# Performance work log

Hardware: AMD Instinct MI355X
Metric: run time of the kernel (lower is better)

Reference implementation:

```python
import jax, jax.numpy as jnp
import numpy as np

N = 100_000            # nodes
E = 1_600_000          # edges (avg degree 16)
IN, OUT = 64, 16
L1, L2 = 48, 32        # in - floor(k*(in-out)/3) for k=1,2
EDGE_DIM = 16
EPS = 1e-7             # GENConv message epsilon
BN_EPS = 1e-5


def _lin(k, i, o):
    return jax.random.normal(k, (i, o), jnp.float32) / np.float32(np.sqrt(i))


def setup_inputs() -> dict:
    key = jax.random.key(0)
    ks = jax.random.split(key, 16)
    z = lambda d: jnp.zeros((d,), jnp.float32)
    o = lambda d: jnp.ones((d,), jnp.float32)
    return {
        "x": jax.random.normal(ks[0], (N, IN), jnp.float32),
        "edge_index": jax.random.randint(ks[1], (2, E), 0, N),
        "edge_attr": jax.random.normal(ks[2], (E, EDGE_DIM), jnp.float32),
        # GENConv 1 (IN -> L1)
        "w_src1": _lin(ks[3], IN, L1), "b_src1": z(L1),
        "w_edge1": _lin(ks[4], EDGE_DIM, L1), "b_edge1": z(L1),
        "w_m1a": _lin(ks[5], L1, 2 * L1), "b_m1a": z(2 * L1),
        "g1": o(2 * L1), "be1": z(2 * L1),
        "w_m1b": _lin(ks[6], 2 * L1, L1), "b_m1b": z(L1),
        # GENConv 2 (L1 -> L2)
        "w_src2": _lin(ks[7], L1, L2), "b_src2": z(L2),
        "w_edge2": _lin(ks[8], EDGE_DIM, L2), "b_edge2": z(L2),
        "w_m2a": _lin(ks[9], L2, 2 * L2), "b_m2a": z(2 * L2),
        "g2": o(2 * L2), "be2": z(2 * L2),
        "w_m2b": _lin(ks[10], 2 * L2, L2), "b_m2b": z(L2),
        # GCNConv heads (L2 -> OUT)
        "w_mu": _lin(ks[11], L2, OUT), "b_mu": z(OUT),
        "w_ls": _lin(ks[12], L2, OUT), "b_ls": z(OUT),
    }


def _gen_conv(x, src, dst, e_raw, w_src, b_src, w_edge, b_edge,
              w1, b1, g, be, w2, b2):
    """PyG GENConv with softmax aggregation (t=1) and 2-layer MLP w/ batch norm."""
    h = x @ w_src + b_src                      # [N, d] lin_src
    e = e_raw @ w_edge + b_edge                # [E, d] lin_edge
    msg = jax.nn.relu(h[src] + e) + EPS        # [E, d] message
    # per-destination, per-channel softmax aggregation
    mmax = jax.ops.segment_max(msg, dst, num_segments=N)
    mmax = jnp.where(jnp.isfinite(mmax), mmax, 0.0)
    ex = jnp.exp(msg - mmax[dst])
    denom = jax.ops.segment_sum(ex, dst, num_segments=N)
    agg = jax.ops.segment_sum(ex * msg, dst, num_segments=N) / (denom + 1e-16)
    out = agg + h                              # residual with x_dst (lin_src applied)
    # MLP: Linear -> BatchNorm(train stats) -> ReLU -> Linear
    zt = out @ w1 + b1
    zt = (zt - zt.mean(0)) * jax.lax.rsqrt(zt.var(0) + BN_EPS) * g + be
    return jax.nn.relu(zt) @ w2 + b2


def _gcn_conv(x, src, dst, w, b):
    """PyG GCNConv: self-loops + symmetric normalization."""
    loop = jnp.arange(N)
    s = jnp.concatenate([src, loop])
    d = jnp.concatenate([dst, loop])
    deg = jax.ops.segment_sum(jnp.ones(s.shape, x.dtype), d, num_segments=N)
    dinv = jnp.where(deg > 0, jax.lax.rsqrt(deg), 0.0)
    norm = (dinv[s] * dinv[d])[:, None]
    return jax.ops.segment_sum((x @ w)[s] * norm, d, num_segments=N) + b


def reference(x, edge_index, edge_attr,
              w_src1, b_src1, w_edge1, b_edge1, w_m1a, b_m1a, g1, be1, w_m1b, b_m1b,
              w_src2, b_src2, w_edge2, b_edge2, w_m2a, b_m2a, g2, be2, w_m2b, b_m2b,
              w_mu, b_mu, w_ls, b_ls):
    src, dst = edge_index[0], edge_index[1]
    h = jax.nn.relu(_gen_conv(x, src, dst, edge_attr, w_src1, b_src1, w_edge1,
                              b_edge1, w_m1a, b_m1a, g1, be1, w_m1b, b_m1b))
    h = jax.nn.relu(_gen_conv(h, src, dst, edge_attr, w_src2, b_src2, w_edge2,
                              b_edge2, w_m2a, b_m2a, g2, be2, w_m2b, b_m2b))
    mu = _gcn_conv(h, src, dst, w_mu, b_mu)
    logstd = _gcn_conv(h, src, dst, w_ls, b_ls)
    return (mu, logstd)
```

## Files before the change

kernel.cpp:

```cpp
#include <hip/hip_runtime.h>
#include <hip/hip_bf16.h>

typedef unsigned int u32;

#define EPS_MSG 1e-7f
#define BN_EPS  1e-5f

template<int I, int O>
__global__ void k_lin(const float* __restrict__ X, const float* __restrict__ W,
                      const float* __restrict__ B, float* __restrict__ Y,
                      int ldY, int n) {
  __shared__ float Wl[I * O];
  __shared__ float Bl[O];
  for (int t = threadIdx.x; t < I * O; t += blockDim.x) Wl[t] = W[t];
  if (threadIdx.x < O) Bl[threadIdx.x] = B[threadIdx.x];
  __syncthreads();
  int i = blockIdx.x * blockDim.x + threadIdx.x;
  if (i >= n) return;
  float acc[O];
#pragma unroll
  for (int c = 0; c < O; c++) acc[c] = Bl[c];
  const float4* xp = (const float4*)(X + (size_t)i * I);
  for (int q = 0; q < I / 4; q++) {
    float4 v = xp[q];
#pragma unroll
    for (int c = 0; c < O; c++) acc[c] += v.x * Wl[(4 * q + 0) * O + c];
#pragma unroll
    for (int c = 0; c < O; c++) acc[c] += v.y * Wl[(4 * q + 1) * O + c];
#pragma unroll
    for (int c = 0; c < O; c++) acc[c] += v.z * Wl[(4 * q + 2) * O + c];
#pragma unroll
    for (int c = 0; c < O; c++) acc[c] += v.w * Wl[(4 * q + 3) * O + c];
  }
  float* y = Y + (size_t)i * ldY;
#pragma unroll
  for (int c = 0; c < O; c++) y[c] = acc[c];
}

__global__ void k_deg(const int* __restrict__ ei, u32* __restrict__ deg, int E) {
  int e = blockIdx.x * blockDim.x + threadIdx.x;
  if (e < E) atomicAdd(&deg[ei[E + e]], 1u);
}

__global__ void k_scan1(const u32* __restrict__ deg, u32* __restrict__ excl,
                        u32* __restrict__ part, int n) {
  __shared__ u32 sm[256];
  int t = threadIdx.x;
  int base = blockIdx.x * 1024 + t * 4;
  u32 v0 = (base + 0 < n) ? deg[base + 0] : 0u;
  u32 v1 = (base + 1 < n) ? deg[base + 1] : 0u;
  u32 v2 = (base + 2 < n) ? deg[base + 2] : 0u;
  u32 v3 = (base + 3 < n) ? deg[base + 3] : 0u;
  u32 tsum = v0 + v1 + v2 + v3;
  sm[t] = tsum;
  __syncthreads();
  for (int o = 1; o < 256; o <<= 1) {
    u32 v = (t >= o) ? sm[t - o] : 0u;
    __syncthreads();
    sm[t] += v;
    __syncthreads();
  }
  u32 tex = sm[t] - tsum;
  if (t == 255) part[blockIdx.x] = sm[255];
  if (base + 0 < n) excl[base + 0] = tex;
  if (base + 1 < n) excl[base + 1] = tex + v0;
  if (base + 2 < n) excl[base + 2] = tex + v0 + v1;
  if (base + 3 < n) excl[base + 3] = tex + v0 + v1 + v2;
}

__global__ void k_scan2(u32* __restrict__ part, int nb) {
  if (threadIdx.x == 0) {
    u32 acc = 0;
    for (int i = 0; i < nb; i++) { u32 v = part[i]; part[i] = acc; acc += v; }
  }
}

__global__ void k_scan3(u32* __restrict__ rowptr, const u32* __restrict__ part,
                        int n, int E) {
  int i = blockIdx.x * blockDim.x + threadIdx.x;
  if (i < n) rowptr[i] += part[i >> 10];
  if (i == 0) rowptr[n] = (u32)E;
}

__global__ void k_slots(const int* __restrict__ ei, const u32* __restrict__ rowptr,
                        u32* __restrict__ cnt, int* __restrict__ csr_src,
                        int* __restrict__ csr_eid, int E) {
  int e = blockIdx.x * blockDim.x + threadIdx.x;
  if (e >= E) return;
  int s = ei[e], d = ei[E + e];
  u32 slot = rowptr[d] + atomicAdd(&cnt[d], 1u);
  csr_src[slot] = s;
  csr_eid[slot] = e;
}

__global__ void k_gather(const int* __restrict__ csr_eid, const float* __restrict__ ea,
                         float* __restrict__ eaperm, int E) {
  int i = blockIdx.x * blockDim.x + threadIdx.x;
  if (i >= E) return;
  int e = csr_eid[i];
  const float4* p = (const float4*)(ea + (size_t)e * 16);
  float4* q = (float4*)(eaperm + (size_t)i * 16);
  float4 a = p[0], b = p[1], c = p[2], d = p[3];
  q[0] = a; q[1] = b; q[2] = c; q[3] = d;
}

__global__ void k_dinv(const u32* __restrict__ deg, float* __restrict__ dinv, int n) {
  int i = blockIdx.x * blockDim.x + threadIdx.x;
  if (i < n) dinv[i] = rsqrtf((float)(deg[i] + 1u));
}

#define EDGE_DOT(A0,A1,A2,A3) (bias + \
  A0.x * wc[0]  + A0.y * wc[1]  + A0.z * wc[2]  + A0.w * wc[3] + \
  A1.x * wc[4]  + A1.y * wc[5]  + A1.z * wc[6]  + A1.w * wc[7] + \
  A2.x * wc[8]  + A2.y * wc[9]  + A2.z * wc[10] + A2.w * wc[11] + \
  A3.x * wc[12] + A3.y * wc[13] + A3.z * wc[14] + A3.w * wc[15])

template<bool PERM>
__global__ void k_agg48(const u32* __restrict__ rowptr, const int* __restrict__ csr_src,
                        const int* __restrict__ csr_eid, const float* __restrict__ attrs,
                        const float* __restrict__ we, const float* __restrict__ be,
                        const float* __restrict__ h, float* __restrict__ out, int n) {
  int lane = threadIdx.x & 63;
  int node = (blockIdx.x * blockDim.x + threadIdx.x) >> 6;
  if (node >= n) return;
  float wc[16];
#pragma unroll
  for (int k = 0; k < 16; k++) wc[k] = 0.f;
  float bias = 0.f;
  if (lane < 48) {
#pragma unroll
    for (int k = 0; k < 16; k++) wc[k] = we[k * 48 + lane];
    bias = be[lane];
  }
  float hself = (lane < 48) ? h[(size_t)node * 48 + lane] : 0.f;
  u32 b = rowptr[node], t = rowptr[node + 1];
  float den = 0.f, num = 0.f;
  u32 i = b;
  if (PERM) {
    for (; i + 4 <= t; i += 4) {
      int s0 = csr_src[i + 0];
      int s1 = csr_src[i + 1];
      int s2 = csr_src[i + 2];
      int s3 = csr_src[i + 3];
      float hv[4];
      if (lane < 48) {
        hv[0] = h[(size_t)s0 * 48 + lane];
        hv[1] = h[(size_t)s1 * 48 + lane];
        hv[2] = h[(size_t)s2 * 48 + lane];
        hv[3] = h[(size_t)s3 * 48 + lane];
      } else { hv[0] = hv[1] = hv[2] = hv[3] = 0.f; }
#pragma unroll
      for (int j = 0; j < 4; j++) {
        const float4* p = (const float4*)(attrs + (size_t)(i + j) * 16);
        float4 a0 = p[0], a1 = p[1], a2 = p[2], a3 = p[3];
        float ml = EDGE_DOT(a0, a1, a2, a3);
        float m  = fmaxf(hv[j] + ml, 0.f) + EPS_MSG;
        float ex = __expf(m);
        den += ex; num += ex * m;
      }
    }
  }
  for (; i < t; i++) {
    int s = csr_src[i];
    const float4* p = (const float4*)(attrs + (PERM ? (size_t)i : (size_t)csr_eid[i]) * 16);
    float4 a0 = p[0], a1 = p[1], a2 = p[2], a3 = p[3];
    float hvs = (lane < 48) ? h[(size_t)s * 48 + lane] : 0.f;
    float ml = EDGE_DOT(a0, a1, a2, a3);
    float m  = fmaxf(hvs + ml, 0.f) + EPS_MSG;
    float ex = __expf(m);
    den += ex; num += ex * m;
  }
  if (lane < 48)
    out[(size_t)node * 48 + lane] = hself + num / (den + 1e-16f);
}

template<bool PERM>
__global__ void k_agg32(const u32* __restrict__ rowptr, const int* __restrict__ csr_src,
                        const int* __restrict__ csr_eid, const float* __restrict__ attrs,
                        const float* __restrict__ we, const float* __restrict__ be,
                        const float* __restrict__ h, float* __restrict__ out, int n) {
  int c    = threadIdx.x & 31;
  int node = (blockIdx.x * blockDim.x + threadIdx.x) >> 5;
  if (node >= n) return;
  float wc[16];
#pragma unroll
  for (int k = 0; k < 16; k++) wc[k] = we[k * 32 + c];
  float bias  = be[c];
  float hself = h[(size_t)node * 32 + c];
  u32 b = rowptr[node], t = rowptr[node + 1];
  float den = 0.f, num = 0.f;
  u32 i = b;
  if (PERM) {
    for (; i + 4 <= t; i += 4) {
      int s0 = csr_src[i + 0];
      int s1 = csr_src[i + 1];
      int s2 = csr_src[i + 2];
      int s3 = csr_src[i + 3];
      float hv[4];
      hv[0] = h[(size_t)s0 * 32 + c];
      hv[1] = h[(size_t)s1 * 32 + c];
      hv[2] = h[(size_t)s2 * 32 + c];
      hv[3] = h[(size_t)s3 * 32 + c];
#pragma unroll
      for (int j = 0; j < 4; j++) {
        const float4* p = (const float4*)(attrs + (size_t)(i + j) * 16);
        float4 a0 = p[0], a1 = p[1], a2 = p[2], a3 = p[3];
        float ml = EDGE_DOT(a0, a1, a2, a3);
        float m  = fmaxf(hv[j] + ml, 0.f) + EPS_MSG;
        float ex = __expf(m);
        den += ex; num += ex * m;
      }
    }
  }
  for (; i < t; i++) {
    int s = csr_src[i];
    const float4* p = (const float4*)(attrs + (PERM ? (size_t)i : (size_t)csr_eid[i]) * 16);
    float4 a0 = p[0], a1 = p[1], a2 = p[2], a3 = p[3];
    float hvs = h[(size_t)s * 32 + c];
    float ml = EDGE_DOT(a0, a1, a2, a3);
    float m  = fmaxf(hvs + ml, 0.f) + EPS_MSG;
    float ex = __expf(m);
    den += ex; num += ex * m;
  }
  out[(size_t)node * 32 + c] = hself + num / (den + 1e-16f);
}

template<int D>
__global__ void k_ztstats(const float* __restrict__ X, const float* __restrict__ W,
                          const float* __restrict__ B, float* __restrict__ Z1,
                          float* __restrict__ Z2, float* __restrict__ partial, int n) {
  __shared__ float Wl[D * 2 * D];
  __shared__ float Bl[2 * D];
  __shared__ float red[4][4 * D];
  for (int t = threadIdx.x; t < D * 2 * D; t += blockDim.x) Wl[t] = W[t];
  for (int t = threadIdx.x; t < 2 * D; t += blockDim.x) Bl[t] = B[t];
  __syncthreads();
  int i = blockIdx.x * blockDim.x + threadIdx.x;
  bool act = (i < n);
  float acc[2 * D];
#pragma unroll
  for (int c = 0; c < 2 * D; c++) acc[c] = 0.f;
  if (act) {
#pragma unroll
    for (int c = 0; c < 2 * D; c++) acc[c] = Bl[c];
    const float4* xp = (const float4*)(X + (size_t)i * D);
    for (int q = 0; q < D / 4; q++) {
      float4 v = xp[q];
#pragma unroll
      for (int c = 0; c < 2 * D; c++) acc[c] += v.x * Wl[(4 * q + 0) * 2 * D + c];
#pragma unroll
      for (int c = 0; c < 2 * D; c++) acc[c] += v.y * Wl[(4 * q + 1) * 2 * D + c];
#pragma unroll
      for (int c = 0; c < 2 * D; c++) acc[c] += v.z * Wl[(4 * q + 2) * 2 * D + c];
#pragma unroll
      for (int c = 0; c < 2 * D; c++) acc[c] += v.w * Wl[(4 * q + 3) * 2 * D + c];
    }
    float* z1 = Z1 + (size_t)i * D;
    float* z2 = Z2 + (size_t)i * D;
#pragma unroll
    for (int c = 0; c < D; c++) { z1[c] = acc[c]; z2[c] = acc[D + c]; }
  } else {
#pragma unroll
    for (int c = 0; c < 2 * D; c++) acc[c] = 0.f;
  }
  int lane = threadIdx.x & 63;
  int wv   = threadIdx.x >> 6;
#pragma unroll
  for (int c = 0; c < 2 * D; c++) {
    float v = acc[c], v2 = v * v;
#pragma unroll
    for (int o = 32; o; o >>= 1) { v += __shfl_xor(v, o); v2 += __shfl_xor(v2, o); }
    if (lane == 0) { red[wv][c] = v; red[wv][2 * D + c] = v2; }
  }
  __syncthreads();
  if (threadIdx.x < 4 * D) {
    float s = red[0][threadIdx.x] + red[1][threadIdx.x] +
              red[2][threadIdx.x] + red[3][threadIdx.x];
    partial[(size_t)blockIdx.x * 4 * D + threadIdx.x] = s;
  }
}

__global__ void k_bnfin(const float* __restrict__ partial, float* __restrict__ stats,
                        int nb, int m) {
  int c = blockIdx.x * blockDim.x + threadIdx.x;
  if (c >= m) return;
  float s = 0.f;
  for (int b = 0; b < nb; b++) s += partial[(size_t)b * m + c];
  stats[c] = s;
}

template<int D, int DD, int O, bool ADDBS>
__global__ void k_mlp_lin(const float* __restrict__ ztA, const float* __restrict__ ztB,
                          const float* __restrict__ stats,
                          const float* __restrict__ G, const float* __restrict__ BE,
                          const float* __restrict__ W2, const float* __restrict__ B2,
                          const float* __restrict__ Wsa, const float* __restrict__ Wsb,
                          const float* __restrict__ Bs,
                          float* __restrict__ out, float invN, int n) {
  __shared__ float Wl[DD * D];
  __shared__ float Ws[D * O];
  __shared__ float Bl[D];
  __shared__ float Bsl[O];
  __shared__ float sc[DD], sh[DD];
  for (int t = threadIdx.x; t < DD * D; t += blockDim.x) Wl[t] = W2[t];
  if (Wsb == nullptr) {
    for (int t = threadIdx.x; t < D * O; t += blockDim.x) Ws[t] = Wsa[t];
  } else {
    for (int t = threadIdx.x; t < D * O; t += blockDim.x) {
      int k = t / O, o = t % O;
      Ws[t] = (o < O / 2) ? Wsa[k * (O / 2) + o] : Wsb[k * (O / 2) + (o - O / 2)];
    }
  }
  if (threadIdx.x < D) Bl[threadIdx.x] = B2[threadIdx.x];
  if (threadIdx.x < O) Bsl[threadIdx.x] = ADDBS ? Bs[threadIdx.x] : 0.f;
  if (threadIdx.x < DD) {
    int c   = threadIdx.x;
    float m = stats[c] * invN;
    float v = stats[DD + c] * invN - m * m;
    float s = G[c] * rsqrtf(v + BN_EPS);
    sc[c] = s; sh[c] = BE[c] - m * s;
  }
  __syncthreads();
  int i = blockIdx.x * blockDim.x + threadIdx.x;
  if (i >= n) return;
  float y[D];
#pragma unroll
  for (int c = 0; c < D; c++) y[c] = Bl[c];
  const float* a = ztA + (size_t)i * D;
  const float* b = ztB + (size_t)i * D;
  for (int k = 0; k < D; k++) {
    float z = fmaxf(a[k] * sc[k] + sh[k], 0.f);
#pragma unroll
    for (int c = 0; c < D; c++) y[c] += z * Wl[k * D + c];
  }
  for (int k = D; k < DD; k++) {
    float z = fmaxf(b[k - D] * sc[k] + sh[k], 0.f);
#pragma unroll
    for (int c = 0; c < D; c++) y[c] += z * Wl[k * D + c];
  }
  float acc[O];
#pragma unroll
  for (int o = 0; o < O; o++) acc[o] = Bsl[o];
#pragma unroll
  for (int k = 0; k < D; k++) {
    float z = fmaxf(y[k], 0.f);
#pragma unroll
    for (int o = 0; o < O; o++) acc[o] += z * Ws[k * O + o];
  }
  float* yo = out + (size_t)i * O;
#pragma unroll
  for (int o = 0; o < O; o++) yo[o] = acc[o];
}

__global__ void k_gcn(const u32* __restrict__ rowptr, const int* __restrict__ csr_src,
                      const float* __restrict__ yz, const float* __restrict__ dinv,
                      const float* __restrict__ bmu, const float* __restrict__ bls,
                      float* __restrict__ out, int n) {
  int c    = threadIdx.x & 31;
  int node = (blockIdx.x * blockDim.x + threadIdx.x) >> 5;
  if (node >= n) return;
  u32 b = rowptr[node], t = rowptr[node + 1];
  float acc = 0.f;
  u32 i = b;
  for (; i + 4 <= t; i += 4) {
    int s0 = csr_src[i + 0];
    int s1 = csr_src[i + 1];
    int s2 = csr_src[i + 2];
    int s3 = csr_src[i + 3];
    float y0 = yz[(size_t)s0 * 32 + c];
    float y1 = yz[(size_t)s1 * 32 + c];
    float y2 = yz[(size_t)s2 * 32 + c];
    float y3 = yz[(size_t)s3 * 32 + c];
    float d0 = dinv[s0], d1 = dinv[s1], d2 = dinv[s2], d3 = dinv[s3];
    acc += y0 * d0 + y1 * d1 + y2 * d2 + y3 * d3;
  }
  for (; i < t; i++) {
    int s0 = csr_src[i];
    acc += yz[(size_t)s0 * 32 + c] * dinv[s0];
  }
  float dv  = dinv[node];
  float val = (acc + yz[(size_t)node * 32 + c] * dv) * dv +
              ((c < 16) ? bmu[c] : bls[c - 16]);
  if (c < 16) out[(size_t)node * 16 + c] = val;
  else        out[(size_t)n * 16 + (size_t)node * 16 + (c - 16)] = val;
}

extern "C" void kernel_launch(void* const* d_in, const int* in_sizes, int n_in,
                              void* d_out, int out_size, void* d_ws, size_t ws_size,
                              hipStream_t stream) {
  const float* x      = (const float*)d_in[0];
  const int*  ei      = (const int*)d_in[1];
  const float* ea     = (const float*)d_in[2];
  const float* w_src1 = (const float*)d_in[3];  const float* b_src1 = (const float*)d_in[4];
  const float* w_edge1= (const float*)d_in[5];  const float* b_edge1= (const float*)d_in[6];
  const float* w_m1a  = (const float*)d_in[7];  const float* b_m1a  = (const float*)d_in[8];
  const float* g1     = (const float*)d_in[9];  const float* be1    = (const float*)d_in[10];
  const float* w_m1b  = (const float*)d_in[11]; const float* b_m1b  = (const float*)d_in[12];
  const float* w_src2 = (const float*)d_in[13]; const float* b_src2 = (const float*)d_in[14];
  const float* w_edge2= (const float*)d_in[15]; const float* b_edge2= (const float*)d_in[16];
  const float* w_m2a  = (const float*)d_in[17]; const float* b_m2a  = (const float*)d_in[18];
  const float* g2     = (const float*)d_in[19]; const float* be2    = (const float*)d_in[20];
  const float* w_m2b  = (const float*)d_in[21]; const float* b_m2b  = (const float*)d_in[22];
  const float* w_mu   = (const float*)d_in[23]; const float* b_mu   = (const float*)d_in[24];
  const float* w_ls   = (const float*)d_in[25]; const float* b_ls   = (const float*)d_in[26];

  const int N = in_sizes[0] / 64;
  const int E = in_sizes[1] / 2;

  const int NB  = (N + 255) / 256;
  const int EB  = (E + 255) / 256;
  const int SB1 = (N + 1023) / 1024;

  float* ws     = (float*)d_ws;
  size_t N48    = (size_t)N * 48;
  float* P0     = ws;
  float* P1     = ws + N48;
  float* P2     = ws + 2 * N48;
  float* P3     = ws + 3 * N48;
  size_t o      = 4 * N48;
  u32*  rowptr  = (u32*)(ws + o);
  u32*  cnt     = rowptr + (N + 1);
  u32*  deg     = cnt + N;
  u32*  part    = deg + N;
  float* dinv   = (float*)(part + 256);
  float* stats  = dinv + N;
  size_t po     = o + 4 * (size_t)N + 769;
  float* partial= ws + po;
  size_t co     = (po + (size_t)NB * 192 + 3) & ~(size_t)3;
  int*  csr_src = (int*)(ws + co);
  int*  csr_eid = csr_src + E;
  size_t eo     = co + 2 * (size_t)E;
  float* eaperm = ws + eo;
  size_t needB  = (eo + 16 * (size_t)E + 16) * sizeof(float);
  const bool PERM = (ws_size >= needB);

  dim3 b256(256);

  hipMemsetAsync(cnt, 0, 2 * (size_t)N * sizeof(u32), stream);

  k_deg<<<EB, b256, 0, stream>>>(ei, deg, E);
  k_scan1<<<SB1, b256, 0, stream>>>(deg, rowptr, part, N);
  k_scan2<<<1, 64, 0, stream>>>(part, SB1);
  k_scan3<<<NB, b256, 0, stream>>>(rowptr, part, N, E);
  k_slots<<<EB, b256, 0, stream>>>(ei, rowptr, cnt, csr_src, csr_eid, E);
  if (PERM) k_gather<<<EB, b256, 0, stream>>>(csr_eid, ea, eaperm, E);
  k_dinv<<<NB, b256, 0, stream>>>(deg, dinv, N);

  const float* attrs = PERM ? eaperm : ea;

  k_lin<64, 48><<<NB, b256, 0, stream>>>(x, w_src1, b_src1, P0, 48, N);
  if (PERM) k_agg48<true><<<(N * 64 + 255) / 256, b256, 0, stream>>>(rowptr, csr_src,
                                           csr_eid, attrs, w_edge1, b_edge1, P0, P3, N);
  else      k_agg48<false><<<(N * 64 + 255) / 256, b256, 0, stream>>>(rowptr, csr_src,
                                           csr_eid, attrs, w_edge1, b_edge1, P0, P3, N);
  k_ztstats<48><<<NB, b256, 0, stream>>>(P3, w_m1a, b_m1a, P1, P2, partial, N);
  k_bnfin<<<1, 256, 0, stream>>>(partial, stats, NB, 192);
  k_mlp_lin<48, 96, 32, true><<<NB, b256, 0, stream>>>(P1, P2, stats, g1, be1,
                                                       w_m1b, b_m1b, w_src2, nullptr,
                                                       b_src2, P0, 1.0f / (float)N, N);

  if (PERM) k_agg32<true><<<(N * 32 + 255) / 256, b256, 0, stream>>>(rowptr, csr_src,
                                           csr_eid, attrs, w_edge2, b_edge2, P0, P3, N);
  else      k_agg32<false><<<(N * 32 + 255) / 256, b256, 0, stream>>>(rowptr, csr_src,
                                           csr_eid, attrs, w_edge2, b_edge2, P0, P3, N);
  k_ztstats<32><<<NB, b256, 0, stream>>>(P3, w_m2a, b_m2a, P1, P2, partial, N);
  k_bnfin<<<1, 256, 0, stream>>>(partial, stats + 256, NB, 128);
  k_mlp_lin<32, 64, 32, false><<<NB, b256, 0, stream>>>(P1, P2, stats + 256, g2, be2,
                                                        w_m2b, b_m2b, w_mu, w_ls,
                                                        nullptr, P0, 1.0f / (float)N, N);

  k_gcn<<<(N * 32 + 255) / 256, b256, 0, stream>>>(rowptr, csr_src, P0, dinv,
                                                   b_mu, b_ls, (float*)d_out, N);
}
```

Before: 1.085 ms.

## Store edge attributes and gathered node features in bf16; prescale GCN features by dinv

The permuted edge-attribute buffer is now stored as packed bf16, and the two GENConv layers also write a bf16 copy of the source-node projections. The aggregation kernels read those halved buffers for the random gathers, and their unroll drops from 4 to 2. Separately, a new pre-pass multiplies the GCN features by dinv, so the GCN gather no longer loads dinv per neighbour. This targets memory traffic in the gather-heavy kernels, at the cost of bf16 rounding in the messages, extra bf16 writes, and one additional small kernel.

```diff
diff --git a/kernel.cpp b/kernel.cpp
--- a/kernel.cpp
+++ b/kernel.cpp
@@ -2,14 +2,35 @@
 #include <hip/hip_bf16.h>
 
 typedef unsigned int u32;
+typedef unsigned short u16;
 
 #define EPS_MSG 1e-7f
 #define BN_EPS  1e-5f
 
-template<int I, int O>
+__device__ __forceinline__ u16 f2bf(float f) {
+  u32 u = __float_as_uint(f);
+  return (u16)((u + 0x7FFFu + ((u >> 16) & 1u)) >> 16);
+}
+__device__ __forceinline__ float bflo(u32 v) { return __uint_as_float(v << 16); }
+__device__ __forceinline__ float bfhi(u32 v) { return __uint_as_float(v & 0xFFFF0000u); }
+__device__ __forceinline__ float bf1(u16 v)  { return __uint_as_float(((u32)v) << 16); }
+
+#define DOTBF(V0, V1) (bias + \
+  bflo(V0.x) * wc[0]  + bfhi(V0.x) * wc[1]  + bflo(V0.y) * wc[2]  + bfhi(V0.y) * wc[3] + \
+  bflo(V0.z) * wc[4]  + bfhi(V0.z) * wc[5]  + bflo(V0.w) * wc[6]  + bfhi(V0.w) * wc[7] + \
+  bflo(V1.x) * wc[8]  + bfhi(V1.x) * wc[9]  + bflo(V1.y) * wc[10] + bfhi(V1.y) * wc[11] + \
+  bflo(V1.z) * wc[12] + bfhi(V1.z) * wc[13] + bflo(V1.w) * wc[14] + bfhi(V1.w) * wc[15])
+
+#define EDGE_DOT(A0,A1,A2,A3) (bias + \
+  A0.x * wc[0]  + A0.y * wc[1]  + A0.z * wc[2]  + A0.w * wc[3] + \
+  A1.x * wc[4]  + A1.y * wc[5]  + A1.z * wc[6]  + A1.w * wc[7] + \
+  A2.x * wc[8]  + A2.y * wc[9]  + A2.z * wc[10] + A2.w * wc[11] + \
+  A3.x * wc[12] + A3.y * wc[13] + A3.z * wc[14] + A3.w * wc[15])
+
+template<int I, int O, bool WBF>
 __global__ void k_lin(const float* __restrict__ X, const float* __restrict__ W,
                       const float* __restrict__ B, float* __restrict__ Y,
-                      int ldY, int n) {
+                      u16* __restrict__ Ybf, int ldY, int n) {
   __shared__ float Wl[I * O];
   __shared__ float Bl[O];
   for (int t = threadIdx.x; t < I * O; t += blockDim.x) Wl[t] = W[t];
@@ -35,6 +56,11 @@
   float* y = Y + (size_t)i * ldY;
 #pragma unroll
   for (int c = 0; c < O; c++) y[c] = acc[c];
+  if (WBF) {
+    u16* yb = Ybf + (size_t)i * O;
+#pragma unroll
+    for (int c = 0; c < O; c++) yb[c] = f2bf(acc[c]);
+  }
 }
 
 __global__ void k_deg(const int* __restrict__ ei, u32* __restrict__ deg, int E) {
@@ -94,14 +120,23 @@
 }
 
 __global__ void k_gather(const int* __restrict__ csr_eid, const float* __restrict__ ea,
-                         float* __restrict__ eaperm, int E) {
+                         u32* __restrict__ eaperm, int E) {
   int i = blockIdx.x * blockDim.x + threadIdx.x;
   if (i >= E) return;
   int e = csr_eid[i];
   const float4* p = (const float4*)(ea + (size_t)e * 16);
-  float4* q = (float4*)(eaperm + (size_t)i * 16);
   float4 a = p[0], b = p[1], c = p[2], d = p[3];
-  q[0] = a; q[1] = b; q[2] = c; q[3] = d;
+  uint4* q = (uint4*)(eaperm + (size_t)i * 8);
+  uint4 w0, w1;
+  w0.x = ((u32)f2bf(a.y) << 16) | f2bf(a.x);
+  w0.y = ((u32)f2bf(a.w) << 16) | f2bf(a.z);
+  w0.z = ((u32)f2bf(b.y) << 16) | f2bf(b.x);
+  w0.w = ((u32)f2bf(b.w) << 16) | f2bf(b.z);
+  w1.x = ((u32)f2bf(c.y) << 16) | f2bf(c.x);
+  w1.y = ((u32)f2bf(c.w) << 16) | f2bf(c.z);
+  w1.z = ((u32)f2bf(d.y) << 16) | f2bf(d.x);
+  w1.w = ((u32)f2bf(d.w) << 16) | f2bf(d.z);
+  q[0] = w0; q[1] = w1;
 }
 
 __global__ void k_dinv(const u32* __restrict__ deg, float* __restrict__ dinv, int n) {
@@ -109,17 +144,13 @@
   if (i < n) dinv[i] = rsqrtf((float)(deg[i] + 1u));
 }
 
-#define EDGE_DOT(A0,A1,A2,A3) (bias + \
-  A0.x * wc[0]  + A0.y * wc[1]  + A0.z * wc[2]  + A0.w * wc[3] + \
-  A1.x * wc[4]  + A1.y * wc[5]  + A1.z * wc[6]  + A1.w * wc[7] + \
-  A2.x * wc[8]  + A2.y * wc[9]  + A2.z * wc[10] + A2.w * wc[11] + \
-  A3.x * wc[12] + A3.y * wc[13] + A3.z * wc[14] + A3.w * wc[15])
-
 template<bool PERM>
 __global__ void k_agg48(const u32* __restrict__ rowptr, const int* __restrict__ csr_src,
-                        const int* __restrict__ csr_eid, const float* __restrict__ attrs,
+                        const int* __restrict__ csr_eid, const u32* __restrict__ eaperm,
+                        const float* __restrict__ ea,
                         const float* __restrict__ we, const float* __restrict__ be,
-                        const float* __restrict__ h, float* __restrict__ out, int n) {
+                        const float* __restrict__ h, const u16* __restrict__ hbf,
+                        float* __restrict__ out, int n) {
   int lane = threadIdx.x & 63;
   int node = (blockIdx.x * blockDim.x + threadIdx.x) >> 6;
   if (node >= n) return;
@@ -137,38 +168,44 @@
   float den = 0.f, num = 0.f;
   u32 i = b;
   if (PERM) {
-    for (; i + 4 <= t; i += 4) {
+    for (; i + 2 <= t; i += 2) {
       int s0 = csr_src[i + 0];
       int s1 = csr_src[i + 1];
-      int s2 = csr_src[i + 2];
-      int s3 = csr_src[i + 3];
-      float hv[4];
-      if (lane < 48) {
-        hv[0] = h[(size_t)s0 * 48 + lane];
-        hv[1] = h[(size_t)s1 * 48 + lane];
-        hv[2] = h[(size_t)s2 * 48 + lane];
-        hv[3] = h[(size_t)s3 * 48 + lane];
-      } else { hv[0] = hv[1] = hv[2] = hv[3] = 0.f; }
-#pragma unroll
-      for (int j = 0; j < 4; j++) {
-        const float4* p = (const float4*)(attrs + (size_t)(i + j) * 16);
-        float4 a0 = p[0], a1 = p[1], a2 = p[2], a3 = p[3];
-        float ml = EDGE_DOT(a0, a1, a2, a3);
-        float m  = fmaxf(hv[j] + ml, 0.f) + EPS_MSG;
-        float ex = __expf(m);
-        den += ex; num += ex * m;
-      }
-    }
-  }
-  for (; i < t; i++) {
-    int s = csr_src[i];
-    const float4* p = (const float4*)(attrs + (PERM ? (size_t)i : (size_t)csr_eid[i]) * 16);
-    float4 a0 = p[0], a1 = p[1], a2 = p[2], a3 = p[3];
-    float hvs = (lane < 48) ? h[(size_t)s * 48 + lane] : 0.f;
-    float ml = EDGE_DOT(a0, a1, a2, a3);
-    float m  = fmaxf(hvs + ml, 0.f) + EPS_MSG;
-    float ex = __expf(m);
-    den += ex; num += ex * m;
+      const uint4* pa = (const uint4*)(eaperm + (size_t)i * 8);
+      uint4 a0 = pa[0], a1 = pa[1];
+      uint4 b0 = pa[2], b1 = pa[3];
+      float h0 = (lane < 48) ? bf1(hbf[(size_t)s0 * 48 + lane]) : 0.f;
+      float h1 = (lane < 48) ? bf1(hbf[(size_t)s1 * 48 + lane]) : 0.f;
+      float ml0 = DOTBF(a0, a1);
+      float ml1 = DOTBF(b0, b1);
+      float m0 = fmaxf(h0 + ml0, 0.f) + EPS_MSG;
+      float m1 = fmaxf(h1 + ml1, 0.f) + EPS_MSG;
+      float ex0 = __expf(m0);
+      float ex1 = __expf(m1);
+      den += ex0 + ex1;
+      num += ex0 * m0 + ex1 * m1;
+    }
+    for (; i < t; i++) {
+      int s = csr_src[i];
+      const uint4* pa = (const uint4*)(eaperm + (size_t)i * 8);
+      uint4 a0 = pa[0], a1 = pa[1];
+      float hv = (lane < 48) ? bf1(hbf[(size_t)s * 48 + lane]) : 0.f;
+      float ml = DOTBF(a0, a1);
+      float m  = fmaxf(hv + ml, 0.f) + EPS_MSG;
+      float ex = __expf(m);
+      den += ex; num += ex * m;
+    }
+  } else {
+    for (; i < t; i++) {
+      int s = csr_src[i];
+      const float4* p = (const float4*)(ea + (size_t)csr_eid[i] * 16);
+      float4 a0 = p[0], a1 = p[1], a2 = p[2], a3 = p[3];
+      float hv = (lane < 48) ? h[(size_t)s * 48 + lane] : 0.f;
+      float ml = EDGE_DOT(a0, a1, a2, a3);
+      float m  = fmaxf(hv + ml, 0.f) + EPS_MSG;
+      float ex = __expf(m);
+      den += ex; num += ex * m;
+    }
   }
   if (lane < 48)
     out[(size_t)node * 48 + lane] = hself + num / (den + 1e-16f);
@@ -176,9 +213,11 @@
 
 template<bool PERM>
 __global__ void k_agg32(const u32* __restrict__ rowptr, const int* __restrict__ csr_src,
-                        const int* __restrict__ csr_eid, const float* __restrict__ attrs,
+                        const int* __restrict__ csr_eid, const u32* __restrict__ eaperm,
+                        const float* __restrict__ ea,
                         const float* __restrict__ we, const float* __restrict__ be,
-                        const float* __restrict__ h, float* __restrict__ out, int n) {
+                        const float* __restrict__ h, const u16* __restrict__ hbf,
+                        float* __restrict__ out, int n) {
   int c    = threadIdx.x & 31;
   int node = (blockIdx.x * blockDim.x + threadIdx.x) >> 5;
   if (node >= n) return;
@@ -191,36 +230,44 @@
   float den = 0.f, num = 0.f;
   u32 i = b;
   if (PERM) {
-    for (; i + 4 <= t; i += 4) {
+    for (; i + 2 <= t; i += 2) {
       int s0 = csr_src[i + 0];
       int s1 = csr_src[i + 1];
-      int s2 = csr_src[i + 2];
-      int s3 = csr_src[i + 3];
-      float hv[4];
-      hv[0] = h[(size_t)s0 * 32 + c];
-      hv[1] = h[(size_t)s1 * 32 + c];
-      hv[2] = h[(size_t)s2 * 32 + c];
-      hv[3] = h[(size_t)s3 * 32 + c];
-#pragma unroll
-      for (int j = 0; j < 4; j++) {
-        const float4* p = (const float4*)(attrs + (size_t)(i + j) * 16);
-        float4 a0 = p[0], a1 = p[1], a2 = p[2], a3 = p[3];
-        float ml = EDGE_DOT(a0, a1, a2, a3);
-        float m  = fmaxf(hv[j] + ml, 0.f) + EPS_MSG;
-        float ex = __expf(m);
-        den += ex; num += ex * m;
-      }
-    }
-  }
-  for (; i < t; i++) {
-    int s = csr_src[i];
-    const float4* p = (const float4*)(attrs + (PERM ? (size_t)i : (size_t)csr_eid[i]) * 16);
-    float4 a0 = p[0], a1 = p[1], a2 = p[2], a3 = p[3];
-    float hvs = h[(size_t)s * 32 + c];
-    float ml = EDGE_DOT(a0, a1, a2, a3);
-    float m  = fmaxf(hvs + ml, 0.f) + EPS_MSG;
-    float ex = __expf(m);
-    den += ex; num += ex * m;
+      const uint4* pa = (const uint4*)(eaperm + (size_t)i * 8);
+      uint4 a0 = pa[0], a1 = pa[1];
+      uint4 b0 = pa[2], b1 = pa[3];
+      float h0 = bf1(hbf[(size_t)s0 * 32 + c]);
+      float h1 = bf1(hbf[(size_t)s1 * 32 + c]);
+      float ml0 = DOTBF(a0, a1);
+      float ml1 = DOTBF(b0, b1);
+      float m0 = fmaxf(h0 + ml0, 0.f) + EPS_MSG;
+      float m1 = fmaxf(h1 + ml1, 0.f) + EPS_MSG;
+      float ex0 = __expf(m0);
+      float ex1 = __expf(m1);
+      den += ex0 + ex1;
+      num += ex0 * m0 + ex1 * m1;
+    }
+    for (; i < t; i++) {
+      int s = csr_src[i];
+      const uint4* pa = (const uint4*)(eaperm + (size_t)i * 8);
+      uint4 a0 = pa[0], a1 = pa[1];
+      float hv = bf1(hbf[(size_t)s * 32 + c]);
+      float ml = DOTBF(a0, a1);
+      float m  = fmaxf(hv + ml, 0.f) + EPS_MSG;
+      float ex = __expf(m);
+      den += ex; num += ex * m;
+    }
+  } else {
+    for (; i < t; i++) {
+      int s = csr_src[i];
+      const float4* p = (const float4*)(ea + (size_t)csr_eid[i] * 16);
+      float4 a0 = p[0], a1 = p[1], a2 = p[2], a3 = p[3];
+      float hv = h[(size_t)s * 32 + c];
+      float ml = EDGE_DOT(a0, a1, a2, a3);
+      float m  = fmaxf(hv + ml, 0.f) + EPS_MSG;
+      float ex = __expf(m);
+      den += ex; num += ex * m;
+    }
   }
   out[(size_t)node * 32 + c] = hself + num / (den + 1e-16f);
 }
@@ -289,14 +336,15 @@
   stats[c] = s;
 }
 
-template<int D, int DD, int O, bool ADDBS>
+template<int D, int DD, int O, bool ADDBS, bool WBF>
 __global__ void k_mlp_lin(const float* __restrict__ ztA, const float* __restrict__ ztB,
                           const float* __restrict__ stats,
                           const float* __restrict__ G, const float* __restrict__ BE,
                           const float* __restrict__ W2, const float* __restrict__ B2,
                           const float* __restrict__ Wsa, const float* __restrict__ Wsb,
                           const float* __restrict__ Bs,
-                          float* __restrict__ out, float invN, int n) {
+                          float* __restrict__ out, u16* __restrict__ outbf,
+                          float invN, int n) {
   __shared__ float Wl[DD * D];
   __shared__ float Ws[D * O];
   __shared__ float Bl[D];
@@ -350,10 +398,22 @@
   float* yo = out + (size_t)i * O;
 #pragma unroll
   for (int o = 0; o < O; o++) yo[o] = acc[o];
+  if (WBF) {
+    u16* yb = outbf + (size_t)i * O;
+#pragma unroll
+    for (int o = 0; o < O; o++) yb[o] = f2bf(acc[o]);
+  }
+}
+
+__global__ void k_scale(const float* __restrict__ yz, const float* __restrict__ dinv,
+                        float* __restrict__ yzd, int n) {
+  int idx = blockIdx.x * blockDim.x + threadIdx.x;
+  if (idx >= n * 32) return;
+  yzd[idx] = yz[idx] * dinv[idx >> 5];
 }
 
 __global__ void k_gcn(const u32* __restrict__ rowptr, const int* __restrict__ csr_src,
-                      const float* __restrict__ yz, const float* __restrict__ dinv,
+                      const float* __restrict__ yzd, const float* __restrict__ dinv,
                       const float* __restrict__ bmu, const float* __restrict__ bls,
                       float* __restrict__ out, int n) {
   int c    = threadIdx.x & 31;
@@ -362,24 +422,16 @@
   u32 b = rowptr[node], t = rowptr[node + 1];
   float acc = 0.f;
   u32 i = b;
-  for (; i + 4 <= t; i += 4) {
-    int s0 = csr_src[i + 0];
+  for (; i + 2 <= t; i += 2) {
+    int s0 = csr_src[i];
     int s1 = csr_src[i + 1];
-    int s2 = csr_src[i + 2];
-    int s3 = csr_src[i + 3];
-    float y0 = yz[(size_t)s0 * 32 + c];
-    float y1 = yz[(size_t)s1 * 32 + c];
-    float y2 = yz[(size_t)s2 * 32 + c];
-    float y3 = yz[(size_t)s3 * 32 + c];
-    float d0 = dinv[s0], d1 = dinv[s1], d2 = dinv[s2], d3 = dinv[s3];
-    acc += y0 * d0 + y1 * d1 + y2 * d2 + y3 * d3;
-  }
-  for (; i < t; i++) {
-    int s0 = csr_src[i];
-    acc += yz[(size_t)s0 * 32 + c] * dinv[s0];
-  }
+    float y0 = yzd[(size_t)s0 * 32 + c];
+    float y1 = yzd[(size_t)s1 * 32 + c];
+    acc += y0 + y1;
+  }
+  if (i < t) acc += yzd[(size_t)csr_src[i] * 32 + c];
   float dv  = dinv[node];
-  float val = (acc + yz[(size_t)node * 32 + c] * dv) * dv +
+  float val = (acc + yzd[(size_t)node * 32 + c]) * dv +
               ((c < 16) ? bmu[c] : bls[c - 16]);
   if (c < 16) out[(size_t)node * 16 + c] = val;
   else        out[(size_t)n * 16 + (size_t)node * 16 + (c - 16)] = val;
@@ -430,8 +482,12 @@
   int*  csr_src = (int*)(ws + co);
   int*  csr_eid = csr_src + E;
   size_t eo     = co + 2 * (size_t)E;
-  float* eaperm = ws + eo;
-  size_t needB  = (eo + 16 * (size_t)E + 16) * sizeof(float);
+  u32*  eaperm  = (u32*)(ws + eo);
+  size_t ho     = eo + 8 * (size_t)E;
+  u16*  hbf1    = (u16*)(ws + ho);
+  size_t h2o    = ho + 24 * (size_t)N;
+  u16*  hbf2    = (u16*)(ws + h2o);
+  size_t needB  = (h2o + 16 * (size_t)N + 16) * sizeof(float);
   const bool PERM = (ws_size >= needB);
 
   dim3 b256(256);
@@ -446,29 +502,31 @@
   if (PERM) k_gather<<<EB, b256, 0, stream>>>(csr_eid, ea, eaperm, E);
   k_dinv<<<NB, b256, 0, stream>>>(deg, dinv, N);
 
-  const float* attrs = PERM ? eaperm : ea;
-
-  k_lin<64, 48><<<NB, b256, 0, stream>>>(x, w_src1, b_src1, P0, 48, N);
+  if (PERM) k_lin<64, 48, true><<<NB, b256, 0, stream>>>(x, w_src1, b_src1, P0, hbf1, 48, N);
+  else      k_lin<64, 48, false><<<NB, b256, 0, stream>>>(x, w_src1, b_src1, P0, nullptr, 48, N);
   if (PERM) k_agg48<true><<<(N * 64 + 255) / 256, b256, 0, stream>>>(rowptr, csr_src,
-                                           csr_eid, attrs, w_edge1, b_edge1, P0, P3, N);
+                       csr_eid, eaperm, ea, w_edge1, b_edge1, P0, hbf1, P3, N);
   else      k_agg48<false><<<(N * 64 + 255) / 256, b256, 0, stream>>>(rowptr, csr_src,
-                                           csr_eid, attrs, w_edge1, b_edge1, P0, P3, N);
+                       csr_eid, eaperm, ea, w_edge1, b_edge1, P0, hbf1, P3, N);
   k_ztstats<48><<<NB, b256, 0, stream>>>(P3, w_m1a, b_m1a, P1, P2, partial, N);
   k_bnfin<<<1, 256, 0, stream>>>(partial, stats, NB, 192);
-  k_mlp_lin<48, 96, 32, true><<<NB, b256, 0, stream>>>(P1, P2, stats, g1, be1,
-                                                       w_m1b, b_m1b, w_src2, nullptr,
-                                                       b_src2, P0, 1.0f / (float)N, N);
+  if (PERM)
+    k_mlp_lin<48, 96, 32, true, true><<<NB, b256, 0, stream>>>(P1, P2, stats, g1, be1,
+                       w_m1b, b_m1b, w_src2, nullptr, b_src2, P0, hbf2, 1.0f / (float)N, N);
+  else
+    k_mlp_lin<48, 96, 32, true, false><<<NB, b256, 0, stream>>>(P1, P2, stats, g1, be1,
+                       w_m1b, b_m1b, w_src2, nullptr, b_src2, P0, nullptr, 1.0f / (float)N, N);
 
   if (PERM) k_agg32<true><<<(N * 32 + 255) / 256, b256, 0, stream>>>(rowptr, csr_src,
-                                           csr_eid, attrs, w_edge2, b_edge2, P0, P3, N);
+                       csr_eid, eaperm, ea, w_edge2, b_edge2, P0, hbf2, P3, N);
   else      k_agg32<false><<<(N * 32 + 255) / 256, b256, 0, stream>>>(rowptr, csr_src,
-                                           csr_eid, attrs, w_edge2, b_edge2, P0, P3, N);
+                       csr_eid, eaperm, ea, w_edge2, b_edge2, P0, hbf2, P3, N);
   k_ztstats<32><<<NB, b256, 0, stream>>>(P3, w_m2a, b_m2a, P1, P2, partial, N);
   k_bnfin<<<1, 256, 0, stream>>>(partial, stats + 256, NB, 128);
-  k_mlp_lin<32, 64, 32, false><<<NB, b256, 0, stream>>>(P1, P2, stats + 256, g2, be2,
-                                                        w_m2b, b_m2b, w_mu, w_ls,
-                                                        nullptr, P0, 1.0f / (float)N, N);
-
-  k_gcn<<<(N * 32 + 255) / 256, b256, 0, stream>>>(rowptr, csr_src, P0, dinv,
+  k_mlp_lin<32, 64, 32, false, false><<<NB, b256, 0, stream>>>(P1, P2, stats + 256, g2, be2,
+                       w_m2b, b_m2b, w_mu, w_ls, nullptr, P0, nullptr, 1.0f / (float)N, N);
+
+  k_scale<<<(N * 32 + 255) / 256, b256, 0, stream>>>(P0, dinv, P3, N);
+  k_gcn<<<(N * 32 + 255) / 256, b256, 0, stream>>>(rowptr, csr_src, P3, dinv,
                                                    b_mu, b_ls, (float*)d_out, N);
 }
```

Result: faster. 1.009 ms (-7.1%).
